# Optimization experiments

Hardware: AMD Instinct MI355X
Metric: run time of the kernel (lower is better)

Reference implementation:

```python
import jax, jax.numpy as jnp
import numpy as np

D_MODEL = 768
D_INNER = 1536
D_STATE = 16
D_CONV = 4
DT_RANK = 48
N_LAYER = 4
VOCAB = 32000
B, L = 2, 1024


def rmsnorm(x, w, eps=1e-5):
    return x * jax.lax.rsqrt(jnp.mean(x * x, axis=-1, keepdims=True) + eps) * w


def depthwise_causal_conv(u, w):
    # u: (b, l, d_in), w: (d_in, k). torch pads both sides then truncates to l,
    # which equals left-pad by k-1 (causal).
    b, l, d = u.shape
    k = w.shape[1]
    up = jnp.pad(u, ((0, 0), (k - 1, 0), (0, 0)))
    out = jnp.zeros_like(u)
    for i in range(k):
        out = out + up[:, i:i + l, :] * w[:, i]
    return out


def selective_scan(u, delta, A, Bm, C, Dp):
    # u,delta: (b,l,d_in); A: (d_in,n); Bm,C: (b,l,n); Dp: (d_in,)
    dA = jnp.exp(delta[..., None] * A)                      # (b,l,d,n)
    dBu = delta[..., None] * Bm[:, :, None, :] * u[..., None]

    def step(h, inp):
        dA_t, dBu_t, C_t = inp
        h = dA_t * h + dBu_t                                 # (b,d,n)
        y = jnp.einsum('bdn,bn->bd', h, C_t)
        return h, y

    h0 = jnp.zeros_like(dA[:, 0])
    xs = (jnp.moveaxis(dA, 1, 0), jnp.moveaxis(dBu, 1, 0), jnp.moveaxis(C, 1, 0))
    _, ys = jax.lax.scan(step, h0, xs)                       # (l,b,d)
    return jnp.moveaxis(ys, 0, 1) + u * Dp


def setup_inputs() -> dict:
    key = jax.random.key(0)
    ks = jax.random.split(key, 16)
    s = lambda fan: 1.0 / np.sqrt(fan)
    inp = {}
    inp['text_input'] = jax.random.randint(ks[0], (B, L), 0, VOCAB)
    inp['visual_input'] = jax.random.normal(ks[1], (B, L, D_MODEL), dtype=jnp.float32)
    inp['embedding'] = jax.random.normal(ks[2], (VOCAB, D_MODEL), dtype=jnp.float32) * 0.02
    inp['norm_w'] = jnp.ones((N_LAYER, D_MODEL), dtype=jnp.float32)
    inp['norm_f_w'] = jnp.ones((D_MODEL,), dtype=jnp.float32)
    inp['in_proj_w'] = jax.random.normal(ks[3], (N_LAYER, 2 * D_INNER, D_MODEL)) * s(D_MODEL)
    inp['in_proj2_w'] = jax.random.normal(ks[4], (N_LAYER, D_INNER, D_MODEL)) * s(D_MODEL)
    inp['conv_w'] = jax.random.normal(ks[5], (N_LAYER, D_INNER, D_CONV)) * s(D_CONV)
    inp['conv_b'] = jax.random.normal(ks[6], (N_LAYER, D_INNER)) * 0.01
    inp['x_proj_w'] = jax.random.normal(ks[7], (N_LAYER, DT_RANK + D_STATE, D_INNER)) * s(D_INNER)
    inp['c_proj_w'] = jax.random.normal(ks[8], (N_LAYER, D_STATE, D_INNER)) * s(D_INNER)
    inp['dt_proj_w'] = jax.random.normal(ks[9], (N_LAYER, D_INNER, DT_RANK)) * s(DT_RANK)
    inp['dt_proj_b'] = jax.random.normal(ks[10], (N_LAYER, D_INNER)) * 0.01
    A = jnp.tile(jnp.arange(1, D_STATE + 1, dtype=jnp.float32)[None, :], (D_INNER, 1))
    inp['A_log'] = jnp.tile(jnp.log(A)[None], (N_LAYER, 1, 1))
    inp['D'] = jnp.ones((N_LAYER, D_INNER), dtype=jnp.float32)
    inp['out_proj_w'] = jax.random.normal(ks[11], (N_LAYER, D_MODEL, D_INNER)) * s(D_INNER)
    return inp


def reference(text_input, visual_input, embedding, norm_w, norm_f_w, in_proj_w,
              in_proj2_w, conv_w, conv_b, x_proj_w, c_proj_w, dt_proj_w,
              dt_proj_b, A_log, D, out_proj_w):
    x = embedding[text_input]  # (b,l,d_model)
    n_layer = A_log.shape[0]
    l = x.shape[1]
    for i in range(n_layer):
        q = rmsnorm(x, norm_w[i])
        v = rmsnorm(visual_input, norm_w[i])
        xr = q @ in_proj_w[i].T                               # (b,l,2*d_inner)
        vin = v @ in_proj2_w[i].T                             # (b,l,d_inner)
        t, res = jnp.split(xr, 2, axis=-1)
        t = depthwise_causal_conv(t, conv_w[i]) + conv_b[i]
        t = jax.nn.silu(t)
        # ssm
        A = -jnp.exp(A_log[i])
        x_dbl = t @ x_proj_w[i].T                             # (b,l,dt_rank+n)
        delta, Bm = jnp.split(x_dbl, [DT_RANK], axis=-1)
        C = vin @ c_proj_w[i].T                               # (b,l,n)
        delta = jax.nn.softplus(delta @ dt_proj_w[i].T + dt_proj_b[i])
        y = selective_scan(t, delta, A, Bm, C, D[i])
        y = y * jax.nn.silu(res)
        x = y @ out_proj_w[i].T + x
    x = rmsnorm(x, norm_f_w)
    return x @ embedding.T  # tied lm_head -> (b,l,vocab)
```

## Files before the change

kernel.cpp:

```cpp
#include <hip/hip_runtime.h>
#include <hip/hip_bf16.h>
#include <math.h>

#define B_ 2
#define L_ 1024
#define DM 768
#define DI 1536
#define DS 16
#define DR 48
#define NL 4
#define VOC 32000
#define BL (B_*L_)
#define NCH 32
#define LCH (L_/NCH)
#define NXD 80
#define DTILE 8

typedef __attribute__((ext_vector_type(8))) short short8;
typedef __attribute__((ext_vector_type(4))) float f32x4;

__device__ __forceinline__ float sigmoidf_(float x){ return 1.f/(1.f+expf(-x)); }
__device__ __forceinline__ float siluf_(float x){ return x*sigmoidf_(x); }
__device__ __forceinline__ float softplusf_(float x){ return fmaxf(x,0.f) + log1pf(expf(-fabsf(x))); }
__device__ __forceinline__ unsigned short f2bf(float f){
    unsigned u = __float_as_uint(f);
    u += 0x7FFFu + ((u >> 16) & 1u);
    return (unsigned short)(u >> 16);
}
__device__ __forceinline__ float bf2f(unsigned short h){
    return __uint_as_float((unsigned)h << 16);
}
__device__ __forceinline__ void gload_lds16(const unsigned short* g, unsigned short* l){
    __builtin_amdgcn_global_load_lds(
        (const __attribute__((address_space(1))) void*)g,
        (__attribute__((address_space(3))) void*)l, 16, 0, 0);
}

__global__ void cast_bf16_kernel(const float* __restrict__ in, unsigned short* __restrict__ out, int n4)
{
    for (int i = blockIdx.x*256 + threadIdx.x; i < n4; i += gridDim.x*256) {
        float4 v = ((const float4*)in)[i];
        ushort4 o;
        o.x = f2bf(v.x); o.y = f2bf(v.y); o.z = f2bf(v.z); o.w = f2bf(v.w);
        ((ushort4*)out)[i] = o;
    }
}

__global__ void embed_kernel(const int* __restrict__ idx, const float* __restrict__ emb,
                             float* __restrict__ x)
{
    int i = blockIdx.x*256 + threadIdx.x;
    if (i >= BL*DM) return;
    int c = i % DM; int bl = i / DM;
    x[i] = emb[(size_t)idx[bl]*DM + c];
}

__global__ void rmsnorm_bf_kernel(const float* __restrict__ in, const float* __restrict__ w,
                                  unsigned short* __restrict__ out)
{
    int row = blockIdx.x;
    const float* xr = in + (size_t)row*DM;
    float ss = 0.f;
    for (int c = threadIdx.x; c < DM; c += 256) { float v = xr[c]; ss += v*v; }
    #pragma unroll
    for (int o = 32; o > 0; o >>= 1) ss += __shfl_down(ss, o, 64);
    __shared__ float red[4];
    if ((threadIdx.x & 63) == 0) red[threadIdx.x >> 6] = ss;
    __syncthreads();
    float tot = red[0] + red[1] + red[2] + red[3];
    float scale = rsqrtf(tot * (1.f/DM) + 1e-5f);
    for (int c = threadIdx.x; c < DM; c += 256)
        out[(size_t)row*DM + c] = f2bf(xr[c]*scale*w[c]);
}

__global__ void prep_layer(
    const float* __restrict__ x, const float* __restrict__ vis, const float* __restrict__ w,
    unsigned short* __restrict__ qh, unsigned short* __restrict__ ql,
    unsigned short* __restrict__ vh, unsigned short* __restrict__ vl,
    const float* __restrict__ s1, unsigned short* __restrict__ h1, unsigned short* __restrict__ l1, int n1,
    const float* __restrict__ s2, unsigned short* __restrict__ h2, unsigned short* __restrict__ l2, int n2,
    const float* __restrict__ s3, unsigned short* __restrict__ h3, unsigned short* __restrict__ l3, int n3)
{
    if (blockIdx.x < 2*BL) {
        int row = blockIdx.x;
        bool first = row < BL;
        int r = first ? row : row - BL;
        const float* xr = (first ? x : vis) + (size_t)r*DM;
        unsigned short* oh = (first ? qh : vh) + (size_t)r*DM;
        unsigned short* ol = (first ? ql : vl) + (size_t)r*DM;
        float ss = 0.f;
        for (int c = threadIdx.x; c < DM; c += 256) { float v = xr[c]; ss += v*v; }
        #pragma unroll
        for (int o = 32; o > 0; o >>= 1) ss += __shfl_down(ss, o, 64);
        __shared__ float red[4];
        if ((threadIdx.x & 63) == 0) red[threadIdx.x >> 6] = ss;
        __syncthreads();
        float tot = red[0] + red[1] + red[2] + red[3];
        float scale = rsqrtf(tot * (1.f/DM) + 1e-5f);
        for (int c = threadIdx.x; c < DM; c += 256) {
            float v = xr[c]*scale*w[c];
            unsigned short h = f2bf(v);
            oh[c] = h;
            ol[c] = f2bf(v - bf2f(h));
        }
    } else {
        int total = n1 + n2 + n3;
        int nblk = gridDim.x - 2*BL;
        for (int i = (blockIdx.x - 2*BL)*256 + threadIdx.x; i < total; i += nblk*256) {
            const float* s; unsigned short *h, *l; int j;
            if (i < n1)           { s = s1; h = h1; l = l1; j = i; }
            else if (i < n1 + n2) { s = s2; h = h2; l = l2; j = i - n1; }
            else                  { s = s3; h = h3; l = l3; j = i - n1 - n2; }
            float4 v = ((const float4*)s)[j];
            ushort4 hh, ll;
            hh.x = f2bf(v.x); ll.x = f2bf(v.x - bf2f(hh.x));
            hh.y = f2bf(v.y); ll.y = f2bf(v.y - bf2f(hh.y));
            hh.z = f2bf(v.z); ll.z = f2bf(v.z - bf2f(hh.z));
            hh.w = f2bf(v.w); ll.w = f2bf(v.w - bf2f(hh.w));
            ((ushort4*)h)[j] = hh;
            ((ushort4*)l)[j] = ll;
        }
    }
}

__global__ __launch_bounds__(512) void gemm_head8(
    const unsigned short* __restrict__ A, int lda,
    const unsigned short* __restrict__ W, int ldb,
    float* __restrict__ C, int ldc, int K)
{
    __shared__ unsigned short As[2][256*64];
    __shared__ unsigned short Bs[2][256*64];
    const int tid = threadIdx.x;
    const int bm = blockIdx.y*256, bn = blockIdx.x*256;
    const int l  = tid & 63;
    const int w  = tid >> 6;
    const int wm = w >> 2, wn = w & 3;
    const int lr = l & 15, lg = l >> 4;

    auto stage = [&](int t, int db) {
        int k0 = t*64;
        #pragma unroll
        for (int i = 0; i < 4; i++) {
            int c = i*512 + tid;
            int row = c >> 3, kb = c & 7;
            int kbs = (kb ^ (row & 7)) << 3;
            gload_lds16(A + (size_t)(bm+row)*lda + k0 + kbs, &As[db][c*8]);
        }
        #pragma unroll
        for (int i = 0; i < 4; i++) {
            int c = i*512 + tid;
            int row = c >> 3, kb = c & 7;
            int kbs = (kb ^ (row & 7)) << 3;
            gload_lds16(W + (size_t)(bn+row)*ldb + k0 + kbs, &Bs[db][c*8]);
        }
    };

    f32x4 zero4 = {0.f, 0.f, 0.f, 0.f};
    f32x4 acc[8][4];
    #pragma unroll
    for (int m = 0; m < 8; m++)
        #pragma unroll
        for (int n = 0; n < 4; n++) acc[m][n] = zero4;

    const int NT = K/64;
    stage(0, 0);
    stage(1, 1);

    for (int t = 0; t < NT; t++) {
        int cur = t & 1;
        if (t + 1 < NT) { asm volatile("s_waitcnt vmcnt(8)" ::: "memory"); }
        else            { asm volatile("s_waitcnt vmcnt(0)" ::: "memory"); }
        __builtin_amdgcn_s_barrier();
        __builtin_amdgcn_sched_barrier(0);

        const unsigned short* Ab = As[cur];
        const unsigned short* Bb = Bs[cur];
        short8 bf0[4], bf1[4];
        #pragma unroll
        for (int n = 0; n < 4; n++) {
            int row = wn*64 + n*16 + lr;
            bf0[n] = *(const short8*)&Bb[row*64 + ((lg       ^ (row & 7)) << 3)];
            bf1[n] = *(const short8*)&Bb[row*64 + (((4 + lg) ^ (row & 7)) << 3)];
        }
        #pragma unroll
        for (int m = 0; m < 8; m++) {
            int row = wm*128 + m*16 + lr;
            short8 a0 = *(const short8*)&Ab[row*64 + ((lg       ^ (row & 7)) << 3)];
            short8 a1 = *(const short8*)&Ab[row*64 + (((4 + lg) ^ (row & 7)) << 3)];
            __builtin_amdgcn_s_setprio(1);
            #pragma unroll
            for (int n = 0; n < 4; n++) {
                acc[m][n] = __builtin_amdgcn_mfma_f32_16x16x32_bf16(a0, bf0[n], acc[m][n], 0, 0, 0);
                acc[m][n] = __builtin_amdgcn_mfma_f32_16x16x32_bf16(a1, bf1[n], acc[m][n], 0, 0, 0);
            }
            __builtin_amdgcn_s_setprio(0);
        }
        __builtin_amdgcn_sched_barrier(0);
        __builtin_amdgcn_s_barrier();
        if (t + 2 < NT) stage(t + 2, cur);
    }

    #pragma unroll
    for (int m = 0; m < 8; m++)
        #pragma unroll
        for (int n = 0; n < 4; n++) {
            int col = bn + wn*64 + n*16 + lr;
            #pragma unroll
            for (int r = 0; r < 4; r++) {
                int rowi = bm + wm*128 + m*16 + lg*4 + r;
                C[(size_t)rowi*ldc + col] = acc[m][n][r];
            }
        }
}

template<int EPI>
__device__ __forceinline__ void mfma2_body(
    const unsigned short* __restrict__ Ah, const unsigned short* __restrict__ Alo, int lda,
    const unsigned short* __restrict__ Wh, const unsigned short* __restrict__ Wlo, int ldb,
    float* __restrict__ C, int ldc, const float* __restrict__ extra,
    int K, int bm, int bn,
    unsigned short* Ash, unsigned short* Asl, unsigned short* Bsh, unsigned short* Bsl)
{
    const int tid = threadIdx.x;
    const int l  = tid & 63;
    const int w  = tid >> 6;
    const int wr = (w >> 1)*64, wc = (w & 1)*64;
    const int lr = l & 15, lg = l >> 4;

    f32x4 zero4 = {0.f, 0.f, 0.f, 0.f};
    f32x4 acc[4][4];
    #pragma unroll
    for (int m = 0; m < 4; m++)
        #pragma unroll
        for (int n = 0; n < 4; n++) acc[m][n] = zero4;

    for (int k0 = 0; k0 < K; k0 += 64) {
        __syncthreads();
        #pragma unroll
        for (int i = 0; i < 4; i++) {
            int c   = i*256 + tid;
            int row = c >> 3;
            int kb  = c & 7;
            int kbs = (kb ^ (row & 7)) << 3;
            const size_t ao = (size_t)(bm+row)*lda + k0 + kbs;
            const size_t bo = (size_t)(bn+row)*ldb + k0 + kbs;
            gload_lds16(Ah  + ao, &Ash[c*8]);
            gload_lds16(Alo + ao, &Asl[c*8]);
            gload_lds16(Wh  + bo, &Bsh[c*8]);
            gload_lds16(Wlo + bo, &Bsl[c*8]);
        }
        __syncthreads();
        #pragma unroll
        for (int kk = 0; kk < 2; kk++) {
            short8 ah[4], al[4], bh[4], bl[4];
            #pragma unroll
            for (int m = 0; m < 4; m++) {
                int row = wr + m*16 + lr;
                int so  = row*64 + (((kk*4 + lg) ^ (row & 7)) << 3);
                ah[m] = *(const short8*)&Ash[so];
                al[m] = *(const short8*)&Asl[so];
            }
            #pragma unroll
            for (int n = 0; n < 4; n++) {
                int row = wc + n*16 + lr;
                int so  = row*64 + (((kk*4 + lg) ^ (row & 7)) << 3);
                bh[n] = *(const short8*)&Bsh[so];
                bl[n] = *(const short8*)&Bsl[so];
            }
            #pragma unroll
            for (int m = 0; m < 4; m++)
                #pragma unroll
                for (int n = 0; n < 4; n++) {
                    acc[m][n] = __builtin_amdgcn_mfma_f32_16x16x32_bf16(al[m], bh[n], acc[m][n], 0, 0, 0);
                    acc[m][n] = __builtin_amdgcn_mfma_f32_16x16x32_bf16(ah[m], bl[n], acc[m][n], 0, 0, 0);
                    acc[m][n] = __builtin_amdgcn_mfma_f32_16x16x32_bf16(ah[m], bh[n], acc[m][n], 0, 0, 0);
                }
        }
    }

    #pragma unroll
    for (int m = 0; m < 4; m++)
        #pragma unroll
        for (int n = 0; n < 4; n++) {
            int col = bn + wc + n*16 + lr;
            #pragma unroll
            for (int r = 0; r < 4; r++) {
                int rowi = bm + wr + m*16 + lg*4 + r;
                float v = acc[m][n][r];
                if (EPI == 1) v += extra[(size_t)rowi*ldc + col];
                C[(size_t)rowi*ldc + col] = v;
            }
        }
}

template<int EPI>
__global__ __launch_bounds__(256) void gemm_mfma2(
    const unsigned short* __restrict__ Ah, const unsigned short* __restrict__ Alo, int lda,
    const unsigned short* __restrict__ Wh, const unsigned short* __restrict__ Wlo, int ldb,
    float* __restrict__ C, int ldc, const float* __restrict__ extra, int K)
{
    __shared__ unsigned short Ash[128*64];
    __shared__ unsigned short Asl[128*64];
    __shared__ unsigned short Bsh[128*64];
    __shared__ unsigned short Bsl[128*64];
    mfma2_body<EPI>(Ah, Alo, lda, Wh, Wlo, ldb, C, ldc, extra, K,
                    blockIdx.y*128, blockIdx.x*128, Ash, Asl, Bsh, Bsl);
}

__global__ __launch_bounds__(256) void gemm_mfma2_dual(
    const unsigned short* __restrict__ Ah1, const unsigned short* __restrict__ Al1,
    const unsigned short* __restrict__ Wh1, const unsigned short* __restrict__ Wl1,
    float* __restrict__ C1, int ldc1, int nb1,
    const unsigned short* __restrict__ Ah2, const unsigned short* __restrict__ Al2,
    const unsigned short* __restrict__ Wh2, const unsigned short* __restrict__ Wl2,
    float* __restrict__ C2, int ldc2,
    int lda, int ldb, int K)
{
    __shared__ unsigned short Ash[128*64];
    __shared__ unsigned short Asl[128*64];
    __shared__ unsigned short Bsh[128*64];
    __shared__ unsigned short Bsl[128*64];
    int bx = blockIdx.x;
    if (bx < nb1)
        mfma2_body<0>(Ah1, Al1, lda, Wh1, Wl1, ldb, C1, ldc1, nullptr, K,
                      blockIdx.y*128, bx*128, Ash, Asl, Bsh, Bsl);
    else
        mfma2_body<0>(Ah2, Al2, lda, Wh2, Wl2, ldb, C2, ldc2, nullptr, K,
                      blockIdx.y*128, (bx-nb1)*128, Ash, Asl, Bsh, Bsl);
}

template<int EPI>
__global__ __launch_bounds__(256) void gemm_tile(
    const float* __restrict__ A, int lda,
    const float* __restrict__ W, int ldb,
    float* __restrict__ C, int ldc,
    const float* __restrict__ extra,
    int K)
{
    __shared__ float As[8][128];
    __shared__ float Bs[8][128];
    const int bm = blockIdx.y * 128;
    const int bn = blockIdx.x * 128;
    const int tid = threadIdx.x;
    const int lr = tid >> 1;
    const int lh = (tid & 1) * 4;
    const int tr = tid >> 4;
    const int tc = tid & 15;

    float acc[8][8];
    #pragma unroll
    for (int i = 0; i < 8; i++)
        #pragma unroll
        for (int j = 0; j < 8; j++) acc[i][j] = 0.f;

    const float* Arow = A + (size_t)(bm + lr)*lda + lh;
    const float* Wrow = W + (size_t)(bn + lr)*ldb + lh;

    for (int k0 = 0; k0 < K; k0 += 8) {
        float4 av = *(const float4*)(Arow + k0);
        float4 wv = *(const float4*)(Wrow + k0);
        __syncthreads();
        As[lh+0][lr] = av.x; As[lh+1][lr] = av.y; As[lh+2][lr] = av.z; As[lh+3][lr] = av.w;
        Bs[lh+0][lr] = wv.x; Bs[lh+1][lr] = wv.y; Bs[lh+2][lr] = wv.z; Bs[lh+3][lr] = wv.w;
        __syncthreads();
        #pragma unroll
        for (int k = 0; k < 8; k++) {
            float a[8], b[8];
            *(float4*)(a)   = *(const float4*)&As[k][tr*8];
            *(float4*)(a+4) = *(const float4*)&As[k][tr*8+4];
            *(float4*)(b)   = *(const float4*)&Bs[k][tc*8];
            *(float4*)(b+4) = *(const float4*)&Bs[k][tc*8+4];
            #pragma unroll
            for (int i = 0; i < 8; i++)
                #pragma unroll
                for (int j = 0; j < 8; j++)
                    acc[i][j] = fmaf(a[i], b[j], acc[i][j]);
        }
    }

    #pragma unroll
    for (int i = 0; i < 8; i++) {
        int row = bm + tr*8 + i;
        float* crow = C + (size_t)row*ldc + bn + tc*8;
        float v[8];
        if (EPI == 2) {
            const float* bia = extra + bn + tc*8;
            #pragma unroll
            for (int j = 0; j < 8; j++) v[j] = softplusf_(acc[i][j] + bia[j]);
        } else {
            #pragma unroll
            for (int j = 0; j < 8; j++) v[j] = acc[i][j];
        }
        *(float4*)(crow)   = make_float4(v[0],v[1],v[2],v[3]);
        *(float4*)(crow+4) = make_float4(v[4],v[5],v[6],v[7]);
    }
}

__global__ __launch_bounds__(256) void gemm_skinny2(
    const float* __restrict__ A1, const float* __restrict__ A2, int lda,
    const float* __restrict__ W1, const float* __restrict__ W2, int ldb,
    float* __restrict__ outx, int K)
{
    __shared__ float As[64][36];
    __shared__ float Ws[16][36];
    int tid = threadIdx.x;
    int bx = blockIdx.x;
    bool isC = (bx == 4);
    const float* A = isC ? A2 : A1;
    const float* W = isC ? W2 : W1;
    int bn = isC ? 0 : bx*16;
    int colbase = isC ? 64 : bx*16;
    int bm = blockIdx.y*64;
    int ar = tid >> 2, ak = (tid & 3)*8;
    int wr = tid >> 4, wk = (tid & 15)*2;
    int tr = tid >> 4, tc = tid & 15;

    float acc[4] = {0.f,0.f,0.f,0.f};
    for (int k0 = 0; k0 < K; k0 += 32) {
        float4 a0 = *(const float4*)(A + (size_t)(bm+ar)*lda + k0 + ak);
        float4 a1 = *(const float4*)(A + (size_t)(bm+ar)*lda + k0 + ak + 4);
        float2 wv = *(const float2*)(W + (size_t)(bn+wr)*ldb + k0 + wk);
        __syncthreads();
        *(float4*)&As[ar][ak]   = a0;
        *(float4*)&As[ar][ak+4] = a1;
        Ws[wr][wk] = wv.x; Ws[wr][wk+1] = wv.y;
        __syncthreads();
        #pragma unroll
        for (int k = 0; k < 32; k += 4) {
            float4 wv4 = *(const float4*)&Ws[tc][k];
            #pragma unroll
            for (int i = 0; i < 4; i++) {
                float4 av4 = *(const float4*)&As[tr*4+i][k];
                acc[i] = fmaf(av4.x, wv4.x, acc[i]);
                acc[i] = fmaf(av4.y, wv4.y, acc[i]);
                acc[i] = fmaf(av4.z, wv4.z, acc[i]);
                acc[i] = fmaf(av4.w, wv4.w, acc[i]);
            }
        }
    }
    #pragma unroll
    for (int i = 0; i < 4; i++)
        outx[(size_t)(bm + tr*4 + i)*NXD + colbase + tc] = acc[i];
}

__global__ void conv_silu_kernel(const float* __restrict__ xr, const float* __restrict__ cw,
                                 const float* __restrict__ cb, float* __restrict__ t)
{
    int i = blockIdx.x*256 + threadIdx.x;
    if (i >= BL*DI) return;
    int d = i % DI; int bl = i / DI; int l = bl % L_; int b = bl / L_;
    const float* base = xr + (size_t)b*L_*(2*DI);
    float acc = cb[d];
    #pragma unroll
    for (int q = 0; q < 4; q++) {
        int ll = l - 3 + q;
        if (ll >= 0) acc = fmaf(base[(size_t)ll*(2*DI) + d], cw[d*4+q], acc);
    }
    t[i] = siluf_(acc);
}

__global__ __launch_bounds__(256) void scan_fused(
    const float* __restrict__ delta, const float* __restrict__ t,
    const float* __restrict__ xdbl,
    const float* __restrict__ A_log, const float* __restrict__ Dp,
    const float* __restrict__ xr,
    unsigned short* __restrict__ zh, unsigned short* __restrict__ zl)
{
    __shared__ float P_lds[256*17];
    __shared__ float S_lds[256*17];
    int blk = blockIdx.x;
    int b  = blk / (DI/DTILE);
    int d0 = (blk % (DI/DTILE))*DTILE;
    int tid = threadIdx.x;
    int dl = tid & (DTILE-1), c = tid / DTILE;
    int d = d0 + dl;

    float Ad[16];
    #pragma unroll
    for (int n = 0; n < 16; n++) Ad[n] = -expf(A_log[d*16+n]);

    float P[16], S[16];
    #pragma unroll
    for (int n = 0; n < 16; n++) { P[n] = 1.f; S[n] = 0.f; }
    for (int s = 0; s < LCH; s++) {
        int bl = b*L_ + c*LCH + s;
        float dt = delta[(size_t)bl*DI + d];
        float u  = t[(size_t)bl*DI + d];
        const float4* Bp4 = (const float4*)(xdbl + (size_t)bl*NXD + 48);
        float Bv[16];
        #pragma unroll
        for (int q = 0; q < 4; q++) {
            float4 bv = Bp4[q];
            Bv[q*4+0]=bv.x; Bv[q*4+1]=bv.y; Bv[q*4+2]=bv.z; Bv[q*4+3]=bv.w;
        }
        float du = dt*u;
        #pragma unroll
        for (int n = 0; n < 16; n++) {
            float a = expf(dt*Ad[n]);
            P[n] *= a;
            S[n] = fmaf(a, S[n], du*Bv[n]);
        }
    }
    #pragma unroll
    for (int n = 0; n < 16; n++) { P_lds[tid*17+n] = P[n]; S_lds[tid*17+n] = S[n]; }
    __syncthreads();

    if (tid < DTILE*16) {
        int dl2 = tid >> 4, n2 = tid & 15;
        float h = 0.f;
        for (int cc = 0; cc < NCH; cc++) {
            int slot = cc*DTILE + dl2;
            float p = P_lds[slot*17 + n2];
            float s = S_lds[slot*17 + n2];
            S_lds[slot*17 + n2] = h;
            h = fmaf(p, h, s);
        }
    }
    __syncthreads();

    float h[16];
    #pragma unroll
    for (int n = 0; n < 16; n++) h[n] = S_lds[tid*17+n];
    float Dd = Dp[d];
    for (int s = 0; s < LCH; s++) {
        int bl = b*L_ + c*LCH + s;
        float dt = delta[(size_t)bl*DI + d];
        float u  = t[(size_t)bl*DI + d];
        const float4* Bp4 = (const float4*)(xdbl + (size_t)bl*NXD + 48);
        const float4* Cp4 = (const float4*)(xdbl + (size_t)bl*NXD + 64);
        float Bv[16], Cv[16];
        #pragma unroll
        for (int q = 0; q < 4; q++) {
            float4 bv = Bp4[q]; float4 cv = Cp4[q];
            Bv[q*4+0]=bv.x; Bv[q*4+1]=bv.y; Bv[q*4+2]=bv.z; Bv[q*4+3]=bv.w;
            Cv[q*4+0]=cv.x; Cv[q*4+1]=cv.y; Cv[q*4+2]=cv.z; Cv[q*4+3]=cv.w;
        }
        float du = dt*u;
        float y = 0.f;
        #pragma unroll
        for (int n = 0; n < 16; n++) {
            float a = expf(dt*Ad[n]);
            h[n] = fmaf(a, h[n], du*Bv[n]);
            y = fmaf(h[n], Cv[n], y);
        }
        y = fmaf(u, Dd, y);
        float r = xr[(size_t)bl*(2*DI) + DI + d];
        float zv = y * siluf_(r);
        unsigned short hh = f2bf(zv);
        zh[(size_t)bl*DI + d] = hh;
        zl[(size_t)bl*DI + d] = f2bf(zv - bf2f(hh));
    }
}

extern "C" void kernel_launch(void* const* d_in, const int* in_sizes, int n_in,
                              void* d_out, int out_size, void* d_ws, size_t ws_size,
                              hipStream_t stream)
{
    const int*   text     = (const int*)  d_in[0];
    const float* visual   = (const float*)d_in[1];
    const float* emb      = (const float*)d_in[2];
    const float* norm_w   = (const float*)d_in[3];
    const float* norm_f_w = (const float*)d_in[4];
    const float* in_proj  = (const float*)d_in[5];
    const float* in_proj2 = (const float*)d_in[6];
    const float* conv_w   = (const float*)d_in[7];
    const float* conv_b   = (const float*)d_in[8];
    const float* x_proj   = (const float*)d_in[9];
    const float* c_proj   = (const float*)d_in[10];
    const float* dt_w     = (const float*)d_in[11];
    const float* dt_b     = (const float*)d_in[12];
    const float* A_log    = (const float*)d_in[13];
    const float* Dp       = (const float*)d_in[14];
    const float* out_proj = (const float*)d_in[15];
    float* out = (float*)d_out;

    float* ws = (float*)d_ws;
    size_t off = 0;
    float* x     = ws + off; off += (size_t)BL*DM;
    float* xr    = ws + off; off += (size_t)BL*2*DI;
    float* vin   = ws + off; off += (size_t)BL*DI;
    float* tb    = ws + off; off += (size_t)BL*DI;
    float* dl    = ws + off; off += (size_t)BL*DI;
    float* xdbl  = ws + off; off += (size_t)BL*NXD;

    unsigned short* bfb = (unsigned short*)(ws + off);
    size_t bo = 0;
    unsigned short* emb_bf = bfb + bo; bo += (size_t)VOC*DM;
    unsigned short* wA_h   = bfb + bo; bo += (size_t)2*DI*DM;
    unsigned short* wA_l   = bfb + bo; bo += (size_t)2*DI*DM;
    unsigned short* wB_h   = bfb + bo; bo += (size_t)DI*DM;
    unsigned short* wB_l   = bfb + bo; bo += (size_t)DI*DM;
    unsigned short* wO_h   = bfb + bo; bo += (size_t)DM*DI;
    unsigned short* wO_l   = bfb + bo; bo += (size_t)DM*DI;
    unsigned short* q_h    = bfb + bo; bo += (size_t)BL*DM;
    unsigned short* q_l    = bfb + bo; bo += (size_t)BL*DM;
    unsigned short* v_h    = bfb + bo; bo += (size_t)BL*DM;
    unsigned short* v_l    = bfb + bo; bo += (size_t)BL*DM;
    unsigned short* z_h    = bfb + bo; bo += (size_t)BL*DI;
    unsigned short* z_l    = bfb + bo; bo += (size_t)BL*DI;
    unsigned short* xn_bf  = bfb + bo; bo += (size_t)BL*DM;

    dim3 blk(256);

    cast_bf16_kernel<<<dim3(2048), blk, 0, stream>>>(emb, emb_bf, VOC*DM/4);

    embed_kernel<<<dim3((BL*DM)/256), blk, 0, stream>>>(text, emb, x);

    for (int i = 0; i < NL; i++) {
        const float* nw = norm_w + (size_t)i*DM;

        prep_layer<<<dim3(2*BL + 1024), blk, 0, stream>>>(
            x, visual, nw, q_h, q_l, v_h, v_l,
            in_proj  + (size_t)i*2*DI*DM, wA_h, wA_l, 2*DI*DM/4,
            in_proj2 + (size_t)i*DI*DM,   wB_h, wB_l, DI*DM/4,
            out_proj + (size_t)i*DM*DI,   wO_h, wO_l, DM*DI/4);

        gemm_mfma2_dual<<<dim3(2*DI/128 + DI/128, BL/128), blk, 0, stream>>>(
            q_h, q_l, wA_h, wA_l, xr, 2*DI, 2*DI/128,
            v_h, v_l, wB_h, wB_l, vin, DI,
            DM, DM, DM);

        conv_silu_kernel<<<dim3((BL*DI)/256), blk, 0, stream>>>(
            xr, conv_w + (size_t)i*DI*4, conv_b + (size_t)i*DI, tb);

        gemm_skinny2<<<dim3(5, BL/64), blk, 0, stream>>>(
            tb, vin, DI, x_proj + (size_t)i*(DR+DS)*DI, c_proj + (size_t)i*DS*DI, DI,
            xdbl, DI);

        gemm_tile<2><<<dim3(DI/128, BL/128), blk, 0, stream>>>(
            xdbl, NXD, dt_w + (size_t)i*DI*DR, DR, dl, DI, dt_b + (size_t)i*DI, DR);

        scan_fused<<<dim3(B_*DI/DTILE), blk, 0, stream>>>(
            dl, tb, xdbl, A_log + (size_t)i*DI*DS, Dp + (size_t)i*DI, xr, z_h, z_l);

        gemm_mfma2<1><<<dim3(DM/128, BL/128), blk, 0, stream>>>(
            z_h, z_l, DI, wO_h, wO_l, DI, x, DM, x, DI);
    }

    rmsnorm_bf_kernel<<<dim3(BL), blk, 0, stream>>>(x, norm_f_w, xn_bf);
    gemm_head8<<<dim3(VOC/256, BL/256), dim3(512), 0, stream>>>(
        xn_bf, DM, emb_bf, DM, out, VOC, DM);
}
```

Measured before the change: 1.588 ms.

## Interleave B-tile prefetch with MFMA phases in the LM-head GEMM

Splits the LM-head GEMM's staging into separate A and B loaders. The next B tile is now issued in two halves between MFMA sub-phases of the current tile, and the A tile follows after the compute loop. The M loop is regrouped into four phases of two row-blocks, each guarded by barriers and an LDS wait. The aim is to spread global-to-LDS traffic across compute instead of bursting it after the loop, at the cost of more workgroup barriers per K step. A small helper for swizzled LDS fragment reads is also factored out.

```diff
diff --git a/kernel.cpp b/kernel.cpp
--- a/kernel.cpp
+++ b/kernel.cpp
@@ -34,6 +34,9 @@
     __builtin_amdgcn_global_load_lds(
         (const __attribute__((address_space(1))) void*)g,
         (__attribute__((address_space(3))) void*)l, 16, 0, 0);
+}
+__device__ __forceinline__ short8 lds_frag(const unsigned short* buf, int row, int kb){
+    return *(const short8*)&buf[row*64 + ((kb ^ (row & 7)) << 3)];
 }
 
 __global__ void cast_bf16_kernel(const float* __restrict__ in, unsigned short* __restrict__ out, int n4)
@@ -137,7 +140,7 @@
     const int wm = w >> 2, wn = w & 3;
     const int lr = l & 15, lg = l >> 4;
 
-    auto stage = [&](int t, int db) {
+    auto stageA = [&](int t, int db) {
         int k0 = t*64;
         #pragma unroll
         for (int i = 0; i < 4; i++) {
@@ -146,9 +149,12 @@
             int kbs = (kb ^ (row & 7)) << 3;
             gload_lds16(A + (size_t)(bm+row)*lda + k0 + kbs, &As[db][c*8]);
         }
-        #pragma unroll
-        for (int i = 0; i < 4; i++) {
-            int c = i*512 + tid;
+    };
+    auto stageB = [&](int t, int db, int half) {
+        int k0 = t*64;
+        #pragma unroll
+        for (int i = 0; i < 2; i++) {
+            int c = (half*2 + i)*512 + tid;
             int row = c >> 3, kb = c & 7;
             int kbs = (kb ^ (row & 7)) << 3;
             gload_lds16(W + (size_t)(bn+row)*ldb + k0 + kbs, &Bs[db][c*8]);
@@ -163,11 +169,12 @@
         for (int n = 0; n < 4; n++) acc[m][n] = zero4;
 
     const int NT = K/64;
-    stage(0, 0);
-    stage(1, 1);
+    stageA(0, 0); stageB(0, 0, 0); stageB(0, 0, 1);
+    stageA(1, 1); stageB(1, 1, 0); stageB(1, 1, 1);
 
     for (int t = 0; t < NT; t++) {
         int cur = t & 1;
+        bool pf = (t + 2) < NT;
         if (t + 1 < NT) { asm volatile("s_waitcnt vmcnt(8)" ::: "memory"); }
         else            { asm volatile("s_waitcnt vmcnt(0)" ::: "memory"); }
         __builtin_amdgcn_s_barrier();
@@ -175,29 +182,43 @@
 
         const unsigned short* Ab = As[cur];
         const unsigned short* Bb = Bs[cur];
+
         short8 bf0[4], bf1[4];
         #pragma unroll
         for (int n = 0; n < 4; n++) {
             int row = wn*64 + n*16 + lr;
-            bf0[n] = *(const short8*)&Bb[row*64 + ((lg       ^ (row & 7)) << 3)];
-            bf1[n] = *(const short8*)&Bb[row*64 + (((4 + lg) ^ (row & 7)) << 3)];
-        }
-        #pragma unroll
-        for (int m = 0; m < 8; m++) {
-            int row = wm*128 + m*16 + lr;
-            short8 a0 = *(const short8*)&Ab[row*64 + ((lg       ^ (row & 7)) << 3)];
-            short8 a1 = *(const short8*)&Ab[row*64 + (((4 + lg) ^ (row & 7)) << 3)];
+            bf0[n] = lds_frag(Bb, row, lg);
+            bf1[n] = lds_frag(Bb, row, 4 + lg);
+        }
+
+        #pragma unroll
+        for (int q = 0; q < 4; q++) {
+            int r0 = wm*128 + (q*2+0)*16 + lr;
+            int r1 = wm*128 + (q*2+1)*16 + lr;
+            short8 a0 = lds_frag(Ab, r0, lg);
+            short8 a1 = lds_frag(Ab, r0, 4 + lg);
+            short8 a2 = lds_frag(Ab, r1, lg);
+            short8 a3 = lds_frag(Ab, r1, 4 + lg);
+            if (pf) {
+                if (q == 1) stageB(t + 2, cur, 0);
+                if (q == 2) stageB(t + 2, cur, 1);
+            }
+            __builtin_amdgcn_s_barrier();
+            asm volatile("s_waitcnt lgkmcnt(0)" ::: "memory");
+            __builtin_amdgcn_sched_barrier(0);
             __builtin_amdgcn_s_setprio(1);
             #pragma unroll
             for (int n = 0; n < 4; n++) {
-                acc[m][n] = __builtin_amdgcn_mfma_f32_16x16x32_bf16(a0, bf0[n], acc[m][n], 0, 0, 0);
-                acc[m][n] = __builtin_amdgcn_mfma_f32_16x16x32_bf16(a1, bf1[n], acc[m][n], 0, 0, 0);
+                acc[q*2+0][n] = __builtin_amdgcn_mfma_f32_16x16x32_bf16(a0, bf0[n], acc[q*2+0][n], 0, 0, 0);
+                acc[q*2+0][n] = __builtin_amdgcn_mfma_f32_16x16x32_bf16(a1, bf1[n], acc[q*2+0][n], 0, 0, 0);
+                acc[q*2+1][n] = __builtin_amdgcn_mfma_f32_16x16x32_bf16(a2, bf0[n], acc[q*2+1][n], 0, 0, 0);
+                acc[q*2+1][n] = __builtin_amdgcn_mfma_f32_16x16x32_bf16(a3, bf1[n], acc[q*2+1][n], 0, 0, 0);
             }
             __builtin_amdgcn_s_setprio(0);
-        }
-        __builtin_amdgcn_sched_barrier(0);
-        __builtin_amdgcn_s_barrier();
-        if (t + 2 < NT) stage(t + 2, cur);
+            __builtin_amdgcn_sched_barrier(0);
+            __builtin_amdgcn_s_barrier();
+        }
+        if (pf) stageA(t + 2, cur);
     }
 
     #pragma unroll
@@ -256,16 +277,14 @@
             #pragma unroll
             for (int m = 0; m < 4; m++) {
                 int row = wr + m*16 + lr;
-                int so  = row*64 + (((kk*4 + lg) ^ (row & 7)) << 3);
-                ah[m] = *(const short8*)&Ash[so];
-                al[m] = *(const short8*)&Asl[so];
+                ah[m] = lds_frag(Ash, row, kk*4 + lg);
+                al[m] = lds_frag(Asl, row, kk*4 + lg);
             }
             #pragma unroll
             for (int n = 0; n < 4; n++) {
                 int row = wc + n*16 + lr;
-                int so  = row*64 + (((kk*4 + lg) ^ (row & 7)) << 3);
-                bh[n] = *(const short8*)&Bsh[so];
-                bl[n] = *(const short8*)&Bsl[so];
+                bh[n] = lds_frag(Bsh, row, kk*4 + lg);
+                bl[n] = lds_frag(Bsl, row, kk*4 + lg);
             }
             #pragma unroll
             for (int m = 0; m < 4; m++)
```

Result: no change. 1.611 ms (+1.5%).

## Replace dual split-bf16 in_proj GEMM with double-buffered 512-thread pipelined kernel

Applied to the files above, without the earlier changes.

Replaces the dual in_proj/in_proj2 GEMM, which used split hi/lo bf16 (three MFMAs per tile), with a new kernel that runs 512 threads (8 waves of 64x32 each) per 128x128 tile. It double-buffers the hi/lo A and B tiles in LDS with async global-to-LDS loads, waiting on vmcnt so the next k-step's loads overlap the current MFMAs. The goal is to hide global load latency and raise per-block wave count. LDS use doubles to 128KB per block, which limits occupancy to one block per CU. It also adds an lds_frag helper for swizzled fragment reads.

```diff
diff --git a/kernel.cpp b/kernel.cpp
--- a/kernel.cpp
+++ b/kernel.cpp
@@ -34,6 +34,9 @@
     __builtin_amdgcn_global_load_lds(
         (const __attribute__((address_space(1))) void*)g,
         (__attribute__((address_space(3))) void*)l, 16, 0, 0);
+}
+__device__ __forceinline__ short8 lds_frag(const unsigned short* buf, int row, int kb){
+    return *(const short8*)&buf[row*64 + ((kb ^ (row & 7)) << 3)];
 }
 
 __global__ void cast_bf16_kernel(const float* __restrict__ in, unsigned short* __restrict__ out, int n4)
@@ -179,14 +182,14 @@
         #pragma unroll
         for (int n = 0; n < 4; n++) {
             int row = wn*64 + n*16 + lr;
-            bf0[n] = *(const short8*)&Bb[row*64 + ((lg       ^ (row & 7)) << 3)];
-            bf1[n] = *(const short8*)&Bb[row*64 + (((4 + lg) ^ (row & 7)) << 3)];
+            bf0[n] = lds_frag(Bb, row, lg);
+            bf1[n] = lds_frag(Bb, row, 4 + lg);
         }
         #pragma unroll
         for (int m = 0; m < 8; m++) {
             int row = wm*128 + m*16 + lr;
-            short8 a0 = *(const short8*)&Ab[row*64 + ((lg       ^ (row & 7)) << 3)];
-            short8 a1 = *(const short8*)&Ab[row*64 + (((4 + lg) ^ (row & 7)) << 3)];
+            short8 a0 = lds_frag(Ab, row, lg);
+            short8 a1 = lds_frag(Ab, row, 4 + lg);
             __builtin_amdgcn_s_setprio(1);
             #pragma unroll
             for (int n = 0; n < 4; n++) {
@@ -208,6 +211,118 @@
             #pragma unroll
             for (int r = 0; r < 4; r++) {
                 int rowi = bm + wm*128 + m*16 + lg*4 + r;
+                C[(size_t)rowi*ldc + col] = acc[m][n][r];
+            }
+        }
+}
+
+__global__ __launch_bounds__(512) void gemm_mfma2p_dual(
+    const unsigned short* __restrict__ Ah1, const unsigned short* __restrict__ Al1,
+    const unsigned short* __restrict__ Wh1, const unsigned short* __restrict__ Wl1,
+    float* __restrict__ C1, int ldc1, int nb1,
+    const unsigned short* __restrict__ Ah2, const unsigned short* __restrict__ Al2,
+    const unsigned short* __restrict__ Wh2, const unsigned short* __restrict__ Wl2,
+    float* __restrict__ C2, int ldc2,
+    int lda, int ldb, int K)
+{
+    __shared__ unsigned short AsH[2][128*64];
+    __shared__ unsigned short AsL[2][128*64];
+    __shared__ unsigned short BsH[2][128*64];
+    __shared__ unsigned short BsL[2][128*64];
+    const int tid = threadIdx.x;
+    const int bx = blockIdx.x;
+    const bool first = bx < nb1;
+    const unsigned short* Ah = first ? Ah1 : Ah2;
+    const unsigned short* Al = first ? Al1 : Al2;
+    const unsigned short* Wh = first ? Wh1 : Wh2;
+    const unsigned short* Wl = first ? Wl1 : Wl2;
+    float* C  = first ? C1 : C2;
+    const int ldc = first ? ldc1 : ldc2;
+    const int bn = (first ? bx : bx - nb1)*128;
+    const int bm = blockIdx.y*128;
+    const int l  = tid & 63;
+    const int w  = tid >> 6;
+    const int wm = w >> 2, wn = w & 3;
+    const int lr = l & 15, lg = l >> 4;
+
+    auto stage = [&](int t, int db) {
+        int k0 = t*64;
+        #pragma unroll
+        for (int i = 0; i < 2; i++) {
+            int c = i*512 + tid;
+            int row = c >> 3, kb = c & 7;
+            int kbs = (kb ^ (row & 7)) << 3;
+            const size_t ao = (size_t)(bm+row)*lda + k0 + kbs;
+            const size_t bo = (size_t)(bn+row)*ldb + k0 + kbs;
+            gload_lds16(Ah + ao, &AsH[db][c*8]);
+            gload_lds16(Al + ao, &AsL[db][c*8]);
+            gload_lds16(Wh + bo, &BsH[db][c*8]);
+            gload_lds16(Wl + bo, &BsL[db][c*8]);
+        }
+    };
+
+    f32x4 zero4 = {0.f, 0.f, 0.f, 0.f};
+    f32x4 acc[4][2];
+    #pragma unroll
+    for (int m = 0; m < 4; m++)
+        #pragma unroll
+        for (int n = 0; n < 2; n++) acc[m][n] = zero4;
+
+    const int NT = K/64;
+    stage(0, 0);
+    stage(1, 1);
+
+    for (int t = 0; t < NT; t++) {
+        int cur = t & 1;
+        if (t + 1 < NT) { asm volatile("s_waitcnt vmcnt(8)" ::: "memory"); }
+        else            { asm volatile("s_waitcnt vmcnt(0)" ::: "memory"); }
+        __builtin_amdgcn_s_barrier();
+        __builtin_amdgcn_sched_barrier(0);
+
+        const unsigned short* AbH = AsH[cur];
+        const unsigned short* AbL = AsL[cur];
+        const unsigned short* BbH = BsH[cur];
+        const unsigned short* BbL = BsL[cur];
+
+        #pragma unroll
+        for (int kk = 0; kk < 2; kk++) {
+            short8 ah[4], al[4], bh[2], bl[2];
+            #pragma unroll
+            for (int m = 0; m < 4; m++) {
+                int row = wm*64 + m*16 + lr;
+                ah[m] = lds_frag(AbH, row, kk*4 + lg);
+                al[m] = lds_frag(AbL, row, kk*4 + lg);
+            }
+            #pragma unroll
+            for (int n = 0; n < 2; n++) {
+                int row = wn*32 + n*16 + lr;
+                bh[n] = lds_frag(BbH, row, kk*4 + lg);
+                bl[n] = lds_frag(BbL, row, kk*4 + lg);
+            }
+            __builtin_amdgcn_s_setprio(1);
+            #pragma unroll
+            for (int m = 0; m < 4; m++)
+                #pragma unroll
+                for (int n = 0; n < 2; n++) {
+                    acc[m][n] = __builtin_amdgcn_mfma_f32_16x16x32_bf16(al[m], bh[n], acc[m][n], 0, 0, 0);
+                    acc[m][n] = __builtin_amdgcn_mfma_f32_16x16x32_bf16(ah[m], bl[n], acc[m][n], 0, 0, 0);
+                    acc[m][n] = __builtin_amdgcn_mfma_f32_16x16x32_bf16(ah[m], bh[n], acc[m][n], 0, 0, 0);
+                }
+            __builtin_amdgcn_s_setprio(0);
+        }
+        __builtin_amdgcn_sched_barrier(0);
+        __builtin_amdgcn_s_barrier();
+        if (t + 2 < NT) stage(t + 2, cur);
+    }
+
+    #pragma unroll
+    for (int m = 0; m < 4; m++)
+        #pragma unroll
+        for (int n = 0; n < 2; n++) {
+            int col = bn + wn*32 + n*16 + lr;
+            #pragma unroll
+            for (int r = 0; r < 4; r++) {
+                int rowi = bm + wm*64 + m*16 + lg*4 + r;
                 C[(size_t)rowi*ldc + col] = acc[m][n][r];
             }
         }
@@ -256,16 +371,14 @@
             #pragma unroll
             for (int m = 0; m < 4; m++) {
                 int row = wr + m*16 + lr;
-                int so  = row*64 + (((kk*4 + lg) ^ (row & 7)) << 3);
-                ah[m] = *(const short8*)&Ash[so];
-                al[m] = *(const short8*)&Asl[so];
+                ah[m] = lds_frag(Ash, row, kk*4 + lg);
+                al[m] = lds_frag(Asl, row, kk*4 + lg);
             }
             #pragma unroll
             for (int n = 0; n < 4; n++) {
                 int row = wc + n*16 + lr;
-                int so  = row*64 + (((kk*4 + lg) ^ (row & 7)) << 3);
-                bh[n] = *(const short8*)&Bsh[so];
-                bl[n] = *(const short8*)&Bsl[so];
+                bh[n] = lds_frag(Bsh, row, kk*4 + lg);
+                bl[n] = lds_frag(Bsl, row, kk*4 + lg);
             }
             #pragma unroll
             for (int m = 0; m < 4; m++)
@@ -305,28 +418,6 @@
     __shared__ unsigned short Bsl[128*64];
     mfma2_body<EPI>(Ah, Alo, lda, Wh, Wlo, ldb, C, ldc, extra, K,
                     blockIdx.y*128, blockIdx.x*128, Ash, Asl, Bsh, Bsl);
-}
-
-__global__ __launch_bounds__(256) void gemm_mfma2_dual(
-    const unsigned short* __restrict__ Ah1, const unsigned short* __restrict__ Al1,
-    const unsigned short* __restrict__ Wh1, const unsigned short* __restrict__ Wl1,
-    float* __restrict__ C1, int ldc1, int nb1,
-    const unsigned short* __restrict__ Ah2, const unsigned short* __restrict__ Al2,
-    const unsigned short* __restrict__ Wh2, const unsigned short* __restrict__ Wl2,
-    float* __restrict__ C2, int ldc2,
-    int lda, int ldb, int K)
-{
-    __shared__ unsigned short Ash[128*64];
-    __shared__ unsigned short Asl[128*64];
-    __shared__ unsigned short Bsh[128*64];
-    __shared__ unsigned short Bsl[128*64];
-    int bx = blockIdx.x;
-    if (bx < nb1)
-        mfma2_body<0>(Ah1, Al1, lda, Wh1, Wl1, ldb, C1, ldc1, nullptr, K,
-                      blockIdx.y*128, bx*128, Ash, Asl, Bsh, Bsl);
-    else
-        mfma2_body<0>(Ah2, Al2, lda, Wh2, Wl2, ldb, C2, ldc2, nullptr, K,
-                      blockIdx.y*128, (bx-nb1)*128, Ash, Asl, Bsh, Bsl);
 }
 
 template<int EPI>
@@ -615,7 +706,7 @@
             in_proj2 + (size_t)i*DI*DM,   wB_h, wB_l, DI*DM/4,
             out_proj + (size_t)i*DM*DI,   wO_h, wO_l, DM*DI/4);
 
-        gemm_mfma2_dual<<<dim3(2*DI/128 + DI/128, BL/128), blk, 0, stream>>>(
+        gemm_mfma2p_dual<<<dim3(2*DI/128 + DI/128, BL/128), dim3(512), 0, stream>>>(
             q_h, q_l, wA_h, wA_l, xr, 2*DI, 2*DI/128,
             v_h, v_l, wB_h, wB_l, vin, DI,
             DM, DM, DM);
```

Measured after the change: 1.589 ms. Within noise of the previous version (+0.0%).
